# Optimization experiments

Measured on AMD Instinct MI355X. Metric: run time of the kernel, lower is better.

The kernel has to match this reference:

```python
import math
import jax, jax.numpy as jnp
import numpy as np

B, T, D, H, NEXP, TOPK = 2, 1024, 1024, 16, 8, 2
DH = D // H
DFF = 4 * D
NEG = -1e30


def _ln(x, g, b, eps=1e-5):
    m = jnp.mean(x, axis=-1, keepdims=True)
    v = jnp.mean((x - m) ** 2, axis=-1, keepdims=True)
    return (x - m) * jax.lax.rsqrt(v + eps) * g + b


def _build_sin_cos(t, dim, base=10000.0):
    # matches torch build_sin_cos(seq_len, head_dim//2): inv freq over range(0, dim*2, 2)
    pos = jnp.arange(t, dtype=jnp.float32)[:, None]
    inv = jnp.exp(jnp.arange(0, dim * 2, 2, dtype=jnp.float32) * (-math.log(base) / (dim * 2)))
    ang = pos * inv  # (T, dim)
    return jnp.sin(ang), jnp.cos(ang)


def _rope(q, k, sin, cos):
    half = q.shape[-1] // 2
    sin = sin[None, :, None, :]
    cos = cos[None, :, None, :]
    q1, q2 = q[..., :half], q[..., half:]
    k1, k2 = k[..., :half], k[..., half:]
    qr = jnp.concatenate([q1 * cos - q2 * sin, q2 * cos + q1 * sin], axis=-1)
    kr = jnp.concatenate([k1 * cos - k2 * sin, k2 * cos + k1 * sin], axis=-1)
    return qr, kr


def _forward(x, noise, ln1_g, ln1_b, ln2_g, ln2_b, w_qkv, w_proj, w_rl, b_rl, w_rn, b_rn, w1, b1, w2, b2):
    # ---- attention sublayer (LN -> RoPE -> causal attn -> proj, residual) ----
    h = _ln(x, ln1_g, ln1_b)
    qkv = (h @ w_qkv).reshape(B, T, 3, H, DH)
    q, k, v = qkv[:, :, 0], qkv[:, :, 1], qkv[:, :, 2]  # (B,T,H,DH)
    sin, cos = _build_sin_cos(T, DH // 2)
    q, k = _rope(q, k, sin, cos)
    scores = jnp.einsum('bthd,bshd->bhts', q, k) / math.sqrt(DH)
    causal = jnp.tril(jnp.ones((T, T), dtype=bool))
    scores = jnp.where(causal[None, None], scores, NEG)
    attn = jax.nn.softmax(scores, axis=-1)
    ao = jnp.einsum('bhts,bshd->bthd', attn, v).reshape(B, T, D)
    x = x + ao @ w_proj
    # ---- MoE sublayer (noisy top-k router -> capped expert dispatch, residual) ----
    h2 = _ln(x, ln2_g, ln2_b).reshape(B * T, D)
    nz = noise.reshape(B * T, NEXP)
    logits = h2 @ w_rl + b_rl
    noisy = logits + nz * jax.nn.softplus(h2 @ w_rn + b_rn)
    topv, ix = jax.lax.top_k(noisy, TOPK)              # (N,K)
    pk = jax.nn.softmax(topv, axis=-1)                 # softmax over sparse (-inf elsewhere)
    route_p = jnp.sum(pk[..., None] * jax.nn.one_hot(ix, NEXP, dtype=pk.dtype), axis=-2)  # (N,E)
    N = B * T
    cap = int(N * TOPK / NEXP)  # capacity per expert (cap_factor=1.0)
    updates = jnp.zeros((N, D), dtype=x.dtype)
    for i in range(NEXP):
        mask = jnp.any(ix == i, axis=-1)               # (N,) tokens routed to expert i
        sel = jnp.argsort(jnp.logical_not(mask))[:cap]  # first `cap` routed tokens, in order (stable sort)
        valid = mask[sel].astype(x.dtype)              # zero out slots beyond actual routed count
        xe = h2[sel]                                   # (cap, D)
        o = jax.nn.relu(xe @ w1[i] + b1[i]) @ w2[i] + b2[i]
        gate = route_p[sel, i] * valid
        updates = updates.at[sel].add(o * gate[:, None])
    return x + updates.reshape(B, T, D)


def setup_inputs() -> dict:
    key = jax.random.key(0)
    ks = jax.random.split(key, 8)
    s = 0.02
    return {
        'x': jax.random.normal(ks[0], (B, T, D), jnp.float32),
        'noise': jax.random.normal(ks[1], (B, T, NEXP), jnp.float32),
        'ln1_g': jnp.ones((D,), jnp.float32),
        'ln1_b': jnp.zeros((D,), jnp.float32),
        'ln2_g': jnp.ones((D,), jnp.float32),
        'ln2_b': jnp.zeros((D,), jnp.float32),
        'w_qkv': jax.random.normal(ks[2], (D, 3 * D), jnp.float32) * s,
        'w_proj': jax.random.normal(ks[3], (D, D), jnp.float32) * s,
        'w_rl': jax.random.normal(ks[4], (D, NEXP), jnp.float32) * s,
        'b_rl': jnp.zeros((NEXP,), jnp.float32),
        'w_rn': jax.random.normal(ks[5], (D, NEXP), jnp.float32) * s,
        'b_rn': jnp.zeros((NEXP,), jnp.float32),
        'w1': jax.random.normal(ks[6], (NEXP, D, DFF), jnp.float32) * s,
        'b1': jnp.zeros((NEXP, DFF), jnp.float32),
        'w2': jax.random.normal(ks[7], (NEXP, DFF, D), jnp.float32) * s,
        'b2': jnp.zeros((NEXP, D), jnp.float32),
    }


def reference(x, noise, ln1_g, ln1_b, ln2_g, ln2_b, w_qkv, w_proj, w_rl, b_rl, w_rn, b_rn, w1, b1, w2, b2):
    return _forward(x, noise, ln1_g, ln1_b, ln2_g, ln2_b, w_qkv, w_proj, w_rl, b_rl, w_rn, b_rn, w1, b1, w2, b2)
```

## Files before the change

### kernel.cpp

```cpp
#include <hip/hip_runtime.h>


#define TB 1024
#define DD 1024
#define NTOK 2048
#define NEXPERT 8
#define CAPN 512
#define DFF 4096

typedef __attribute__((ext_vector_type(4))) float f32x4;
typedef __attribute__((ext_vector_type(16))) float f32x16;
typedef __attribute__((ext_vector_type(8))) short short8;
typedef __attribute__((ext_vector_type(4))) short short4v;
typedef unsigned short u16;
typedef unsigned int u32;

__device__ __forceinline__ u16 f2bf(float f){
  union { float f; u32 u; } v; v.f = f;
  u32 u = v.u;
  u32 r = (u + 0x7fffu + ((u >> 16) & 1u)) >> 16;
  return (u16)r;
}
__device__ __forceinline__ float bf2f(u16 b){
  union { u32 u; float f; } v; v.u = ((u32)b) << 16;
  return v.f;
}
__device__ __forceinline__ float waveRedSum(float v){
#pragma unroll
  for (int o = 1; o < 64; o <<= 1) v += __shfl_xor(v, o);
  return v;
}

__device__ __forceinline__ void gl16(const u16* g, u16* l){
  __builtin_amdgcn_global_load_lds(
    (const __attribute__((address_space(1))) u32*)g,
    (__attribute__((address_space(3))) u32*)l, 16, 0, 0);
}

__global__ __launch_bounds__(256) void k_prep(
    const float* __restrict__ w_qkv, const float* __restrict__ w_proj,
    const float* __restrict__ w1, const float* __restrict__ w2,
    u16* __restrict__ wqkvT, u16* __restrict__ wprojT,
    u16* __restrict__ w1T, u16* __restrict__ w2T,
    float* __restrict__ st, float* __restrict__ ct,
    const float* __restrict__ x, const float* __restrict__ ln1_g,
    const float* __restrict__ ln1_b, u16* __restrict__ h1)
{
  const int tid = threadIdx.x;
  int bid = blockIdx.x;
  if (bid < 128){
    const int idx = bid * 256 + tid;
    const int t = idx >> 5, i = idx & 31;
    const float inv = expf((float)(2 * i) * (-0.14391157f));
    const float ang = (float)t * inv;
    st[idx] = sinf(ang);
    ct[idx] = cosf(ang);
    return;
  }
  bid -= 128;
  if (bid >= 17408){
    const int row = bid - 17408;
    const int w = tid >> 6, lane = tid & 63;
    const float4 xv = *(const float4*)(x + (long)row*DD + tid*4);
    __shared__ float red[8];
    float s = xv.x + xv.y + xv.z + xv.w;
    s = waveRedSum(s);
    if (lane == 0) red[w] = s;
    __syncthreads();
    const float mean = (red[0]+red[1]+red[2]+red[3]) * (1.f/1024.f);
    const float d0 = xv.x-mean, d1 = xv.y-mean, d2 = xv.z-mean, d3 = xv.w-mean;
    float vs = d0*d0 + d1*d1 + d2*d2 + d3*d3;
    vs = waveRedSum(vs);
    if (lane == 0) red[4+w] = vs;
    __syncthreads();
    const float var = (red[4]+red[5]+red[6]+red[7]) * (1.f/1024.f);
    const float inv = rsqrtf(var + 1e-5f);
    const int c = tid*4;
    short4v p;
    p[0] = (short)f2bf(d0*inv*ln1_g[c+0] + ln1_b[c+0]);
    p[1] = (short)f2bf(d1*inv*ln1_g[c+1] + ln1_b[c+1]);
    p[2] = (short)f2bf(d2*inv*ln1_g[c+2] + ln1_b[c+2]);
    p[3] = (short)f2bf(d3*inv*ln1_g[c+3] + ln1_b[c+3]);
    *(short4v*)(h1 + (long)row*DD + c) = p;
    return;
  }
  const float* src; u16* dst; int K, N, nx, tile;
  long zoff = 0;
  if (bid < 768){
    src = w_qkv; dst = wqkvT; K = DD; N = 3*DD; nx = 48; tile = bid;
  } else if (bid < 768 + 256){
    src = w_proj; dst = wprojT; K = DD; N = DD; nx = 16; tile = bid - 768;
  } else if (bid < 768 + 256 + 8192){
    const int b2 = bid - (768 + 256);
    src = w1; dst = w1T; K = DD; N = DFF; nx = 64; tile = b2 & 1023;
    zoff = (long)(b2 >> 10) * DD * DFF;
  } else {
    const int b2 = bid - (768 + 256 + 8192);
    src = w2; dst = w2T; K = DFF; N = DD; nx = 16; tile = b2 & 1023;
    zoff = (long)(b2 >> 10) * DFF * DD;
  }
  const int n0 = (tile % nx) * 64, k0 = (tile / nx) * 64;
  __shared__ float tb[64][65];
  const int r  = tid >> 2;
  const int c4 = (tid & 3) * 16;
#pragma unroll
  for (int j = 0; j < 4; ++j){
    const float4 v = *(const float4*)(src + zoff + (long)(k0 + r)*N + n0 + c4 + j*4);
    tb[r][c4 + j*4 + 0] = v.x;
    tb[r][c4 + j*4 + 1] = v.y;
    tb[r][c4 + j*4 + 2] = v.z;
    tb[r][c4 + j*4 + 3] = v.w;
  }
  __syncthreads();
  const int n  = tid >> 2;
  const int ks = (tid & 3) * 16;
  short8 o0, o1;
#pragma unroll
  for (int j = 0; j < 8; ++j){
    o0[j] = (short)f2bf(tb[ks + j][n]);
    o1[j] = (short)f2bf(tb[ks + 8 + j][n]);
  }
  u16* dp = dst + zoff + (long)k0*N + (long)(n0 + n)*64 + ks;
  *(short8*)dp = o0;
  *(short8*)(dp + 8) = o1;
}

template<bool GATHER>
__device__ __forceinline__ void gemm_core5(
    const u16* __restrict__ A, int lda, const int* __restrict__ rowlist,
    const u16* __restrict__ Bt, int BN, int K, int kstart, int row0, int col0,
    u16* As0, u16* Bs0, u16* As1, u16* Bs1, f32x16 acc[2][2])
{
  const int tid = threadIdx.x;
  const int lane = tid & 63;
  const int w = tid >> 6;
  const int wr = w >> 1, wc = w & 1;
  const int l31 = lane & 31, l5 = lane >> 5;
  const int rr8 = lane >> 3;
  const int cc8 = ((lane & 7) ^ rr8) * 8;

  const u16* Aq[4];
  const u16* Bq[4];
  int coff[4];
#pragma unroll
  for (int j2 = 0; j2 < 4; ++j2){
    const int j = w + 4*j2;
    long ar;
    if constexpr (GATHER) ar = rowlist[row0 + j*8 + rr8];
    else                  ar = row0 + j*8 + rr8;
    Aq[j2] = A + ar*(long)lda + kstart + cc8;
    Bq[j2] = Bt + (long)kstart*BN + (long)(col0 + j*8 + rr8)*64 + cc8;
    coff[j2] = j*512;
  }

  const int swz = (l31 & 7) * 8;

#define STAGE5(AS, BS, KOFF) \
  _Pragma("unroll") \
  for (int j2 = 0; j2 < 4; ++j2){ \
    gl16(Aq[j2] + (KOFF), (AS) + coff[j2]); \
    gl16(Bq[j2] + (long)(KOFF)*BN, (BS) + coff[j2]); \
  }

#define COMPUTE5(AS, BS) \
  _Pragma("unroll") \
  for (int s = 0; s < 4; ++s){ \
    short8 aF[2], bF[2]; \
    const int cread = ((s*16 + l5*8) ^ swz); \
    _Pragma("unroll") \
    for (int mi = 0; mi < 2; ++mi) \
      aF[mi] = *(const short8*)((AS) + (wr*64 + mi*32 + l31)*64 + cread); \
    _Pragma("unroll") \
    for (int ni = 0; ni < 2; ++ni) \
      bF[ni] = *(const short8*)((BS) + (wc*64 + ni*32 + l31)*64 + cread); \
    _Pragma("unroll") \
    for (int mi = 0; mi < 2; ++mi) \
      _Pragma("unroll") \
      for (int ni = 0; ni < 2; ++ni) \
        acc[mi][ni] = __builtin_amdgcn_mfma_f32_32x32x16_bf16(aF[mi], bF[ni], acc[mi][ni], 0, 0, 0); \
  }

  STAGE5(As0, Bs0, 0)

  for (int k0 = 0; k0 < K; k0 += 128){
    STAGE5(As1, Bs1, k0 + 64)
    asm volatile("s_waitcnt vmcnt(8)" ::: "memory");
    __builtin_amdgcn_s_barrier();
    __builtin_amdgcn_sched_barrier(0);
    COMPUTE5(As0, Bs0)
    __builtin_amdgcn_s_barrier();
    if (k0 + 128 < K){
      STAGE5(As0, Bs0, k0 + 128)
      asm volatile("s_waitcnt vmcnt(8)" ::: "memory");
    } else {
      asm volatile("s_waitcnt vmcnt(0)" ::: "memory");
    }
    __builtin_amdgcn_s_barrier();
    __builtin_amdgcn_sched_barrier(0);
    COMPUTE5(As1, Bs1)
    __builtin_amdgcn_s_barrier();
  }
#undef STAGE5
#undef COMPUTE5
}

#define GEMM_PRE4 \
  __shared__ u16 As0[128*64], Bs0[128*64], As1[128*64], Bs1[128*64]; \
  f32x16 acc[2][2]; \
  _Pragma("unroll") for (int i = 0; i < 2; ++i) \
  _Pragma("unroll") for (int j = 0; j < 2; ++j) \
  _Pragma("unroll") for (int q = 0; q < 16; ++q) acc[i][j][q] = 0.f;

#define GEMM_EPI4_VARS \
  const int lane = threadIdx.x & 63; \
  const int wv = threadIdx.x >> 6;   \
  const int wr = wv >> 1, wc = wv & 1; \
  const int l31 = lane & 31, l5 = lane >> 5;

#define ROW4(mi, r) (row0 + wr*64 + (mi)*32 + ((r)&3) + (((r)>>2)<<3) + l5*4)
#define COL4(ni)    (col0 + wc*64 + (ni)*32 + l31)

__global__ __launch_bounds__(256) void k_gemm_qkv(const u16* __restrict__ h1,
    const u16* __restrict__ wqT, const float* __restrict__ st,
    const float* __restrict__ ct, u16* __restrict__ q_r, u16* __restrict__ k_r,
    u16* __restrict__ v_row)
{
  GEMM_PRE4
  const int id = blockIdx.x;
  const int pcol = id % 24, mt = id / 24;
  const int row0 = mt*128, col0 = pcol*128;
  gemm_core5<false>(h1, DD, nullptr, wqT, 3*DD, DD, 0, row0, col0, As0, Bs0, As1, Bs1, acc);
  GEMM_EPI4_VARS
  if (pcol < 16){
    const int isk = pcol >> 3;
    const int h = (pcol & 7)*2 + wc;
    u16* dstbase = isk ? k_r : q_r;
    const float qs = isk ? 1.f : 0.125f;
#pragma unroll
    for (int mi = 0; mi < 2; ++mi)
#pragma unroll
      for (int r = 0; r < 16; ++r){
        const int rr = ROW4(mi, r);
        const int b = rr >> 10, t = rr & (TB-1);
        const float sv = st[t*32 + l31], cv = ct[t*32 + l31];
        const float a0 = acc[mi][0][r], a1 = acc[mi][1][r];
        const float o1 = (a0*cv - a1*sv) * qs;
        const float o2 = (a1*cv + a0*sv) * qs;
        u16* dst = dstbase + ((long)(b*16 + h)*TB + t)*64 + l31;
        dst[0]  = f2bf(o1);
        dst[32] = f2bf(o2);
      }
  } else {
    const int cb = (pcol - 16)*128 + wc*64;
#pragma unroll
    for (int mi = 0; mi < 2; ++mi)
#pragma unroll
      for (int ni = 0; ni < 2; ++ni)
#pragma unroll
        for (int r = 0; r < 16; ++r){
          const int rr = ROW4(mi, r);
          v_row[(long)rr*DD + cb + ni*32 + l31] = f2bf(acc[mi][ni][r]);
        }
  }
}

__global__ __launch_bounds__(256) void k_vt(const u16* __restrict__ v_row,
    u16* __restrict__ v_t)
{
  __shared__ u16 vt[64*72];
  const int tid = threadIdx.x;
  const int bh = blockIdx.y, b = bh >> 4, h = bh & 15;
  const int t0 = blockIdx.x * 64;
  const int tl = tid >> 2, qq = tid & 3;
  const int t = t0 + tl;
  const long row = (long)(b*TB + t) * DD + h*64;
  const short8 w0 = *(const short8*)(v_row + row + qq*16);
  const short8 w1 = *(const short8*)(v_row + row + qq*16 + 8);
#pragma unroll
  for (int j = 0; j < 8; ++j){
    vt[(qq*16 + j)*72 + tl]     = (u16)w0[j];
    vt[(qq*16 + 8 + j)*72 + tl] = (u16)w1[j];
  }
  __syncthreads();
  const int dh = tid >> 2, seg = tid & 3;
  const short8 r0 = *(const short8*)(vt + dh*72 + seg*16);
  const short8 r1 = *(const short8*)(vt + dh*72 + seg*16 + 8);
  u16* vp = v_t + ((long)bh*64 + dh)*TB + t0 + seg*16;
  *(short8*)vp = r0; *(short8*)(vp + 8) = r1;
}

__global__ __launch_bounds__(512) void k_attn(const u16* __restrict__ q_r,
    const u16* __restrict__ k_r, const u16* __restrict__ v_t,
    u16* __restrict__ aoc, float2* __restrict__ mLc)
{
  const int qt = blockIdx.x, bh = blockIdx.y, ch = blockIdx.z;
  const int kvlen = (qt + 1) * 128;
  const int s_begin = ch * 512;
  if (s_begin >= kvlen) return;
  const int ntile = (min(s_begin + 512, kvlen) - s_begin) >> 6;

  __shared__ u16 K_lds[2][64*64];
  __shared__ u16 V_lds[2][64*64];
  __shared__ u16 P_lds[8][16*80];

  const int tid = threadIdx.x;
  const int w = tid >> 6, lane = tid & 63;
  const int l15 = lane & 15, l4 = lane >> 4;
  const int q0 = qt*128 + w*16;
  u16* P = &P_lds[w][0];

  const int srow = tid >> 3, sslot = tid & 7;
  const u16* kq = k_r + ((long)bh*TB + s_begin + srow)*64 + ((sslot ^ (srow & 7))*8);
  const u16* vq = v_t + ((long)bh*64 + srow)*TB + s_begin + ((sslot ^ (srow & 7))*8);
  u16* kD = &K_lds[0][0] + tid*8;
  u16* vD = &V_lds[0][0] + tid*8;

  const long qoff = ((long)bh*TB + q0 + l15)*64 + l4*8;
  const short8 Qf0 = *(const short8*)(q_r + qoff);
  const short8 Qf1 = *(const short8*)(q_r + qoff + 32);
  const f32x4 fz = {0.f,0.f,0.f,0.f};
  f32x4 O[4];
  float m[4], L[4];
#pragma unroll
  for (int i = 0; i < 4; ++i){ O[i] = fz; m[i] = -1e30f; L[i] = 0.f; }

  gl16(kq, kD);
  gl16(vq, vD);

  for (int t = 0; t < ntile; ++t){
    const int s0 = s_begin + t*64;
    const int cur = t & 1;
    if (t + 1 < ntile){
      gl16(kq + (t+1)*4096, kD + (cur^1)*4096);
      gl16(vq + (t+1)*64,   vD + (cur^1)*4096);
      asm volatile("s_waitcnt vmcnt(2)" ::: "memory");
    } else {
      asm volatile("s_waitcnt vmcnt(0)" ::: "memory");
    }
    __builtin_amdgcn_s_barrier();
    __builtin_amdgcn_sched_barrier(0);
    if (s0 <= q0 + 15){
      const u16* Kb = &K_lds[cur][0];
      const u16* Vb = &V_lds[cur][0];
      f32x4 S[4];
#pragma unroll
      for (int sj = 0; sj < 4; ++sj){
        const int rl = sj*16 + l15;
        const short8 kf0 = *(const short8*)(Kb + rl*64 + ((l4 ^ (rl & 7))*8));
        const short8 kf1 = *(const short8*)(Kb + rl*64 + (((l4 + 4) ^ (rl & 7))*8));
        f32x4 z = fz;
        z = __builtin_amdgcn_mfma_f32_16x16x32_bf16(Qf0, kf0, z, 0, 0, 0);
        z = __builtin_amdgcn_mfma_f32_16x16x32_bf16(Qf1, kf1, z, 0, 0, 0);
        S[sj] = z;
      }
      if (s0 + 63 > q0){
#pragma unroll
        for (int sj = 0; sj < 4; ++sj)
#pragma unroll
          for (int r = 0; r < 4; ++r){
            const int sc = s0 + sj*16 + l15;
            const int qr = q0 + l4*4 + r;
            if (sc > qr) S[sj][r] = -1e30f;
          }
      }
      float vm[4];
#pragma unroll
      for (int r = 0; r < 4; ++r){
        vm[r] = fmaxf(fmaxf(S[0][r], S[1][r]), fmaxf(S[2][r], S[3][r]));
        vm[r] = fmaxf(vm[r], __shfl_xor(vm[r], 1));
        vm[r] = fmaxf(vm[r], __shfl_xor(vm[r], 2));
        vm[r] = fmaxf(vm[r], __shfl_xor(vm[r], 4));
        vm[r] = fmaxf(vm[r], __shfl_xor(vm[r], 8));
      }
      float corr[4], ls[4];
#pragma unroll
      for (int r = 0; r < 4; ++r){
        const float mn = fmaxf(m[r], vm[r]);
        corr[r] = __expf(m[r] - mn);
        m[r] = mn;
        ls[r] = 0.f;
      }
#pragma unroll
      for (int sj = 0; sj < 4; ++sj)
#pragma unroll
        for (int r = 0; r < 4; ++r){
          const float pv = __expf(S[sj][r] - m[r]);
          S[sj][r] = pv;
          ls[r] += pv;
        }
#pragma unroll
      for (int r = 0; r < 4; ++r){
        ls[r] += __shfl_xor(ls[r], 1);
        ls[r] += __shfl_xor(ls[r], 2);
        ls[r] += __shfl_xor(ls[r], 4);
        ls[r] += __shfl_xor(ls[r], 8);
        L[r] = L[r]*corr[r] + ls[r];
      }
#pragma unroll
      for (int nj = 0; nj < 4; ++nj)
#pragma unroll
        for (int r = 0; r < 4; ++r)
          O[nj][r] *= corr[r];
#pragma unroll
      for (int sj = 0; sj < 4; ++sj)
#pragma unroll
        for (int r = 0; r < 4; ++r)
          P[(l4*4 + r)*80 + sj*16 + l15] = f2bf(S[sj][r]);
      asm volatile("s_waitcnt lgkmcnt(0)" ::: "memory");
      __builtin_amdgcn_sched_barrier(0);
      const short8 pf0 = *(const short8*)(P + l15*80 + l4*8);
      const short8 pf1 = *(const short8*)(P + l15*80 + 32 + l4*8);
#pragma unroll
      for (int nj = 0; nj < 4; ++nj){
        const int rl = nj*16 + l15;
        const short8 vf0 = *(const short8*)(Vb + rl*64 + ((l4 ^ (rl & 7))*8));
        const short8 vf1 = *(const short8*)(Vb + rl*64 + (((l4 + 4) ^ (rl & 7))*8));
        O[nj] = __builtin_amdgcn_mfma_f32_16x16x32_bf16(pf0, vf0, O[nj], 0, 0, 0);
        O[nj] = __builtin_amdgcn_mfma_f32_16x16x32_bf16(pf1, vf1, O[nj], 0, 0, 0);
      }
    }
    __builtin_amdgcn_sched_barrier(0);
    __builtin_amdgcn_s_barrier();
  }
  const long obase = ((long)(bh*8 + qt)*2 + ch) * 8192;
#pragma unroll
  for (int nj = 0; nj < 4; ++nj)
#pragma unroll
    for (int r = 0; r < 4; ++r)
      aoc[obase + (long)(w*16 + l4*4 + r)*64 + nj*16 + l15] = f2bf(O[nj][r]);
  if (l15 == 0){
#pragma unroll
    for (int r = 0; r < 4; ++r)
      mLc[((long)(bh*8 + qt)*2 + ch)*128 + w*16 + l4*4 + r] = make_float2(m[r], L[r]);
  }
}

__global__ __launch_bounds__(256) void k_attn_comb(const u16* __restrict__ aoc,
    const float2* __restrict__ mLc, u16* __restrict__ ao)
{
  const int bq = blockIdx.x;
  const int qt = bq & 7, bh = bq >> 3, b = bh >> 4, h = bh & 15;
  const int nc2 = (qt >= 4);
  const int d = threadIdx.x & 63;
  const int r0 = threadIdx.x >> 6;
  const long base = (long)bq * 2 * 8192;
  const long mbase = (long)bq * 2 * 128;
  for (int rp = 0; rp < 32; ++rp){
    const int r = rp*4 + r0;
    const float2 ml0 = mLc[mbase + r];
    float o, Lg;
    if (nc2){
      const float2 ml1 = mLc[mbase + 128 + r];
      const float mg = fmaxf(ml0.x, ml1.x);
      const float w0 = __expf(ml0.x - mg), w1 = __expf(ml1.x - mg);
      o  = w0 * bf2f(aoc[base + (long)r*64 + d]) + w1 * bf2f(aoc[base + 8192 + (long)r*64 + d]);
      Lg = w0 * ml0.y + w1 * ml1.y;
    } else {
      o  = bf2f(aoc[base + (long)r*64 + d]);
      Lg = ml0.y;
    }
    const int t = qt*128 + r;
    ao[((long)b*TB + t)*DD + h*64 + d] = f2bf(o / Lg);
  }
}

__global__ __launch_bounds__(256) void k_gemm_proj(const u16* __restrict__ ao,
    const u16* __restrict__ wpT, const float* __restrict__ x, float* __restrict__ out)
{
  GEMM_PRE4
  const int id = blockIdx.x;
  const int pcol = id % 8, mt = id / 8;
  const int row0 = mt*128, col0 = pcol*128;
  gemm_core5<false>(ao, DD, nullptr, wpT, DD, DD, 0, row0, col0, As0, Bs0, As1, Bs1, acc);
  GEMM_EPI4_VARS
#pragma unroll
  for (int mi = 0; mi < 2; ++mi)
#pragma unroll
    for (int ni = 0; ni < 2; ++ni)
#pragma unroll
      for (int r = 0; r < 16; ++r){
        const int rr = ROW4(mi, r);
        const int cc = COL4(ni);
        out[(long)rr*DD + cc] = x[(long)rr*DD + cc] + acc[mi][ni][r];
      }
}

__global__ __launch_bounds__(256) void k_ln2r(const float* __restrict__ x,
    const float* __restrict__ g, const float* __restrict__ bb,
    const float* __restrict__ w_rl, const float* __restrict__ b_rl,
    const float* __restrict__ w_rn, const float* __restrict__ b_rn,
    const float* __restrict__ noise, u16* __restrict__ h2b,
    int2* __restrict__ tok_e, float2* __restrict__ tok_g, int* __restrict__ slot_of)
{
  const int row = blockIdx.x, tid = threadIdx.x;
  const int w = tid >> 6, lane = tid & 63;
  const float4 xv = *(const float4*)(x + (long)row*DD + tid*4);
  __shared__ float red[8];
  __shared__ float red2[4][16];
  float s = xv.x + xv.y + xv.z + xv.w;
  s = waveRedSum(s);
  if (lane == 0) red[w] = s;
  __syncthreads();
  const float mean = (red[0]+red[1]+red[2]+red[3]) * (1.f/1024.f);
  const float d0 = xv.x-mean, d1 = xv.y-mean, d2 = xv.z-mean, d3 = xv.w-mean;
  float vs = d0*d0 + d1*d1 + d2*d2 + d3*d3;
  vs = waveRedSum(vs);
  if (lane == 0) red[4+w] = vs;
  __syncthreads();
  const float var = (red[4]+red[5]+red[6]+red[7]) * (1.f/1024.f);
  const float inv = rsqrtf(var + 1e-5f);
  const int c = tid*4;
  const float hv[4] = {
    d0*inv*g[c+0] + bb[c+0], d1*inv*g[c+1] + bb[c+1],
    d2*inv*g[c+2] + bb[c+2], d3*inv*g[c+3] + bb[c+3]};
  short4v p;
#pragma unroll
  for (int j = 0; j < 4; ++j) p[j] = (short)f2bf(hv[j]);
  *(short4v*)(h2b + (long)row*DD + c) = p;

  float accl[8] = {0,0,0,0,0,0,0,0};
  float accn[8] = {0,0,0,0,0,0,0,0};
#pragma unroll
  for (int j = 0; j < 4; ++j){
    const int k = c + j;
    const float4 a = *(const float4*)(w_rl + k*8);
    const float4 b = *(const float4*)(w_rl + k*8 + 4);
    accl[0] += hv[j]*a.x; accl[1] += hv[j]*a.y; accl[2] += hv[j]*a.z; accl[3] += hv[j]*a.w;
    accl[4] += hv[j]*b.x; accl[5] += hv[j]*b.y; accl[6] += hv[j]*b.z; accl[7] += hv[j]*b.w;
    const float4 cc = *(const float4*)(w_rn + k*8);
    const float4 d = *(const float4*)(w_rn + k*8 + 4);
    accn[0] += hv[j]*cc.x; accn[1] += hv[j]*cc.y; accn[2] += hv[j]*cc.z; accn[3] += hv[j]*cc.w;
    accn[4] += hv[j]*d.x; accn[5] += hv[j]*d.y; accn[6] += hv[j]*d.z; accn[7] += hv[j]*d.w;
  }
#pragma unroll
  for (int e = 0; e < 8; ++e){ accl[e] = waveRedSum(accl[e]); accn[e] = waveRedSum(accn[e]); }
  if (lane == 0){
#pragma unroll
    for (int e = 0; e < 8; ++e){ red2[w][e] = accl[e]; red2[w][8+e] = accn[e]; }
  }
  __syncthreads();
  if (tid == 0){
    float nv[8];
#pragma unroll
    for (int e = 0; e < 8; ++e){
      const float lr = red2[0][e]+red2[1][e]+red2[2][e]+red2[3][e] + b_rl[e];
      const float lnv = red2[0][8+e]+red2[1][8+e]+red2[2][8+e]+red2[3][8+e] + b_rn[e];
      const float sp = fmaxf(lnv, 0.f) + log1pf(expf(-fabsf(lnv)));
      nv[e] = lr + noise[row*8 + e] * sp;
    }
    int bi = 0; float bvv = nv[0];
#pragma unroll
    for (int e = 1; e < 8; ++e) if (nv[e] > bvv){ bvv = nv[e]; bi = e; }
    int si = (bi == 0) ? 1 : 0;
    float sv = nv[si];
#pragma unroll
    for (int e = 0; e < 8; ++e) if (e != bi && nv[e] > sv){ sv = nv[e]; si = e; }
    const float tt = expf(sv - bvv);
    tok_e[row] = make_int2(bi, si);
    tok_g[row] = make_float2(1.f/(1.f + tt), tt/(1.f + tt));
    slot_of[row*2]     = -1;
    slot_of[row*2 + 1] = -1;
  }
}

__global__ __launch_bounds__(256) void k_assign(const int2* __restrict__ tok_e,
    int* __restrict__ expert_tok, int* __restrict__ slot_of)
{
  const int e = blockIdx.x, tid = threadIdx.x;
  __shared__ int cnt[256];
  expert_tok[e*CAPN + tid] = 0;
  expert_tok[e*CAPN + 256 + tid] = 0;
  int which[8]; int c = 0;
  const int t0 = tid * 8;
#pragma unroll
  for (int j = 0; j < 8; ++j){
    const int2 te = tok_e[t0 + j];
    int wj = -1;
    if (te.x == e) wj = 0; else if (te.y == e) wj = 1;
    which[j] = wj;
    c += (wj >= 0) ? 1 : 0;
  }
  cnt[tid] = c;
  __syncthreads();
  if (tid == 0){
    int run = 0;
    for (int i = 0; i < 256; ++i){ const int v = cnt[i]; cnt[i] = run; run += v; }
  }
  __syncthreads();
  int pos = cnt[tid];
#pragma unroll
  for (int j = 0; j < 8; ++j){
    if (which[j] >= 0){
      if (pos < CAPN){
        expert_tok[e*CAPN + pos] = t0 + j;
        slot_of[(t0 + j)*2 + which[j]] = e*CAPN + pos;
      }
      ++pos;
    }
  }
}

__global__ __launch_bounds__(256) void k_ffn1(const u16* __restrict__ h2b,
    const u16* __restrict__ w1T, const float* __restrict__ b1,
    const int* __restrict__ expert_tok, u16* __restrict__ act)
{
  GEMM_PRE4
  const int id = blockIdx.x;
  const int chunk = (id & 7) * 128 + (id >> 3);
  const int mt = chunk & 3, pcol = (chunk >> 2) & 31, z = chunk >> 7;
  const int row0 = mt*128, col0 = pcol*128;
  gemm_core5<true>(h2b, DD, expert_tok + z*CAPN, w1T + (long)z*DD*DFF, DFF, DD, 0,
                   row0, col0, As0, Bs0, As1, Bs1, acc);
  GEMM_EPI4_VARS
#pragma unroll
  for (int mi = 0; mi < 2; ++mi)
#pragma unroll
    for (int ni = 0; ni < 2; ++ni)
#pragma unroll
      for (int r = 0; r < 16; ++r){
        const int rr = ROW4(mi, r);
        const int cc = COL4(ni);
        const float val = fmaxf(acc[mi][ni][r] + b1[z*DFF + cc], 0.f);
        act[((long)z*CAPN + rr)*DFF + cc] = f2bf(val);
      }
}

__global__ __launch_bounds__(256) void k_ffn2(const u16* __restrict__ act,
    const u16* __restrict__ w2T, u16* __restrict__ partial)
{
  GEMM_PRE4
  const int id = blockIdx.x;
  const int chunk = (id & 7) * 64 + (id >> 3);
  const int ks = chunk & 1, mt = (chunk >> 1) & 3, pcol = (chunk >> 3) & 7, z = chunk >> 6;
  const int row0 = mt*128, col0 = pcol*128;
  gemm_core5<false>(act + (long)z*CAPN*DFF, DFF, nullptr,
                    w2T + (long)z*DFF*DD, DD, 2048, ks*2048,
                    row0, col0, As0, Bs0, As1, Bs1, acc);
  GEMM_EPI4_VARS
  u16* pp = partial + (long)ks*NEXPERT*CAPN*DD;
#pragma unroll
  for (int mi = 0; mi < 2; ++mi)
#pragma unroll
    for (int ni = 0; ni < 2; ++ni)
#pragma unroll
      for (int r = 0; r < 16; ++r){
        const int rr = ROW4(mi, r);
        const int cc = COL4(ni);
        pp[((long)z*CAPN + rr)*DD + cc] = f2bf(acc[mi][ni][r]);
      }
}

__global__ __launch_bounds__(256) void k_combine(float* __restrict__ out,
    const int* __restrict__ slot_of, const float2* __restrict__ tok_g,
    const u16* __restrict__ partial, const float* __restrict__ b2)
{
  const int tok = blockIdx.x, c = threadIdx.x * 4;
  float4 o = *(float4*)(out + (long)tok*DD + c);
  const int2 ss = *(const int2*)(slot_of + tok*2);
  const float2 g = tok_g[tok];
#pragma unroll
  for (int j = 0; j < 2; ++j){
    const int s = j ? ss.y : ss.x;
    const float gw = j ? g.y : g.x;
    if (s >= 0){
      const int e = s >> 9;
      float4 a = *(const float4*)(b2 + e*DD + c);
#pragma unroll
      for (int ks = 0; ks < 2; ++ks){
        const short4v pv = *(const short4v*)(partial + (long)ks*NEXPERT*CAPN*DD + (long)s*DD + c);
        a.x += bf2f((u16)pv[0]); a.y += bf2f((u16)pv[1]);
        a.z += bf2f((u16)pv[2]); a.w += bf2f((u16)pv[3]);
      }
      o.x += gw*a.x; o.y += gw*a.y; o.z += gw*a.z; o.w += gw*a.w;
    }
  }
  *(float4*)(out + (long)tok*DD + c) = o;
}

extern "C" void kernel_launch(void* const* d_in, const int* in_sizes, int n_in,
                              void* d_out, int out_size, void* d_ws, size_t ws_size,
                              hipStream_t stream)
{
  (void)in_sizes; (void)n_in; (void)out_size; (void)ws_size;
  const float* x      = (const float*)d_in[0];
  const float* noise  = (const float*)d_in[1];
  const float* ln1_g  = (const float*)d_in[2];
  const float* ln1_b  = (const float*)d_in[3];
  const float* ln2_g  = (const float*)d_in[4];
  const float* ln2_b  = (const float*)d_in[5];
  const float* w_qkv  = (const float*)d_in[6];
  const float* w_proj = (const float*)d_in[7];
  const float* w_rl   = (const float*)d_in[8];
  const float* b_rl   = (const float*)d_in[9];
  const float* w_rn   = (const float*)d_in[10];
  const float* b_rn   = (const float*)d_in[11];
  const float* w1     = (const float*)d_in[12];
  const float* b1     = (const float*)d_in[13];
  const float* w2     = (const float*)d_in[14];
  const float* b2     = (const float*)d_in[15];
  float* out = (float*)d_out;

  char* p = (char*)d_ws;
  auto carve = [&](size_t bytes) -> void* {
    void* r = (void*)p;
    p += (bytes + 255) & ~(size_t)255;
    return r;
  };
  const size_t SLOT = (size_t)NTOK*DD*2;
  float* sin_t      = (float*)carve((size_t)TB*32*4);
  float* cos_t      = (float*)carve((size_t)TB*32*4);
  char*  region     = (char*)carve(SLOT*8);
  u16*   h1    = (u16*)region;
  u16*   v_row = (u16*)(region + SLOT);
  u16*   q_r   = (u16*)(region + SLOT*4);
  u16*   k_r   = (u16*)(region + SLOT*5);
  u16*   v_t   = (u16*)(region + SLOT*6);
  u16*   ao    = (u16*)(region + SLOT*7);
  u16*   aoc   = (u16*)region;
  float2* mLc  = (float2*)(region + SLOT*2);
  u16*   act   = (u16*)region;
  u16*   h2b        = (u16*)  carve((size_t)NTOK*DD*2);
  int2*  tok_e      = (int2*) carve((size_t)NTOK*8);
  float2* tok_g     = (float2*)carve((size_t)NTOK*8);
  int*   slot_of    = (int*)  carve((size_t)NTOK*2*4);
  int*   expert_tok = (int*)  carve((size_t)NEXPERT*CAPN*4);
  u16*   wqkvT      = (u16*)  carve((size_t)DD*3*DD*2);
  u16*   wprojT     = (u16*)  carve((size_t)DD*DD*2);
  u16*   w1T        = (u16*)  carve((size_t)NEXPERT*DD*DFF*2);
  u16*   w2T        = (u16*)  carve((size_t)NEXPERT*DFF*DD*2);
  u16*   partial    = (u16*)w1T;

  k_prep   <<<19584, 256, 0, stream>>>(w_qkv, w_proj, w1, w2,
                                       wqkvT, wprojT, w1T, w2T, sin_t, cos_t,
                                       x, ln1_g, ln1_b, h1);
  k_gemm_qkv<<<384, 256, 0, stream>>>(h1, wqkvT, sin_t, cos_t, q_r, k_r, v_row);
  k_vt     <<<dim3(16, 32), 256, 0, stream>>>(v_row, v_t);
  k_attn   <<<dim3(8, 32, 2), 512, 0, stream>>>(q_r, k_r, v_t, aoc, mLc);
  k_attn_comb<<<256, 256, 0, stream>>>(aoc, mLc, ao);
  k_gemm_proj<<<128, 256, 0, stream>>>(ao, wprojT, x, out);
  k_ln2r   <<<NTOK, 256, 0, stream>>>(out, ln2_g, ln2_b, w_rl, b_rl, w_rn, b_rn,
                                      noise, h2b, tok_e, tok_g, slot_of);
  k_assign <<<NEXPERT, 256, 0, stream>>>(tok_e, expert_tok, slot_of);
  k_ffn1   <<<1024, 256, 0, stream>>>(h2b, w1T, b1, expert_tok, act);
  k_ffn2   <<<512, 256, 0, stream>>>(act, w2T, partial);
  k_combine<<<NTOK, 256, 0, stream>>>(out, slot_of, tok_g, partial, b2);
}
```

Baseline: 312.3 us.

## Widen weight-transpose tiles and convert to bf16 before staging in LDS

The weight prep kernel now transposes 64x256 tiles per block instead of 64x64, cutting the block count from about 19.6k to 6.5k. Each thread converts fp32 to bf16 while loading, so LDS holds u16 values with a padded stride, which halves shared-memory footprint and traffic. The write-out then gathers 8 k-values per output row into 16-byte stores. This aims to lower launch and scheduling overhead and make the large weight conversion pass more bandwidth-efficient. The risk is LDS bank conflicts on 16-bit strided reads and lower occupancy per block.

Result: no change. 312.7 us (+0.1%).

```diff
diff --git a/kernel.cpp b/kernel.cpp
--- a/kernel.cpp
+++ b/kernel.cpp
@@ -58,8 +58,8 @@
     return;
   }
   bid -= 128;
-  if (bid >= 17408){
-    const int row = bid - 17408;
+  if (bid >= 4352){
+    const int row = bid - 4352;
     const int w = tid >> 6, lane = tid & 63;
     const float4 xv = *(const float4*)(x + (long)row*DD + tid*4);
     __shared__ float red[8];
@@ -84,45 +84,46 @@
     *(short4v*)(h1 + (long)row*DD + c) = p;
     return;
   }
-  const float* src; u16* dst; int K, N, nx, tile;
+  const float* src; u16* dst; int N, nnx, tile;
   long zoff = 0;
-  if (bid < 768){
-    src = w_qkv; dst = wqkvT; K = DD; N = 3*DD; nx = 48; tile = bid;
-  } else if (bid < 768 + 256){
-    src = w_proj; dst = wprojT; K = DD; N = DD; nx = 16; tile = bid - 768;
-  } else if (bid < 768 + 256 + 8192){
-    const int b2 = bid - (768 + 256);
-    src = w1; dst = w1T; K = DD; N = DFF; nx = 64; tile = b2 & 1023;
-    zoff = (long)(b2 >> 10) * DD * DFF;
+  if (bid < 192){
+    src = w_qkv; dst = wqkvT; N = 3*DD; nnx = 12; tile = bid;
+  } else if (bid < 256){
+    src = w_proj; dst = wprojT; N = DD; nnx = 4; tile = bid - 192;
+  } else if (bid < 2304){
+    const int b2 = bid - 256;
+    src = w1; dst = w1T; N = DFF; nnx = 16; tile = b2 & 255;
+    zoff = (long)(b2 >> 8) * DD * DFF;
   } else {
-    const int b2 = bid - (768 + 256 + 8192);
-    src = w2; dst = w2T; K = DFF; N = DD; nx = 16; tile = b2 & 1023;
-    zoff = (long)(b2 >> 10) * DFF * DD;
-  }
-  const int n0 = (tile % nx) * 64, k0 = (tile / nx) * 64;
-  __shared__ float tb[64][65];
-  const int r  = tid >> 2;
-  const int c4 = (tid & 3) * 16;
-#pragma unroll
-  for (int j = 0; j < 4; ++j){
-    const float4 v = *(const float4*)(src + zoff + (long)(k0 + r)*N + n0 + c4 + j*4);
-    tb[r][c4 + j*4 + 0] = v.x;
-    tb[r][c4 + j*4 + 1] = v.y;
-    tb[r][c4 + j*4 + 2] = v.z;
-    tb[r][c4 + j*4 + 3] = v.w;
+    const int b2 = bid - 2304;
+    src = w2; dst = w2T; N = DD; nnx = 4; tile = b2 & 255;
+    zoff = (long)(b2 >> 8) * DFF * DD;
+  }
+  const int n0 = (tile % nnx) * 256, k0 = (tile / nnx) * 64;
+
+  __shared__ u16 tb[64*258];
+#pragma unroll
+  for (int i = 0; i < 16; ++i){
+    const int r = i*4 + (tid >> 6);
+    const int c = (tid & 63) * 4;
+    const float4 v = *(const float4*)(src + zoff + (long)(k0 + r)*N + n0 + c);
+    const u32 lo = (u32)f2bf(v.x) | ((u32)f2bf(v.y) << 16);
+    const u32 hi = (u32)f2bf(v.z) | ((u32)f2bf(v.w) << 16);
+    *(u32*)(tb + r*258 + c)     = lo;
+    *(u32*)(tb + r*258 + c + 2) = hi;
   }
   __syncthreads();
-  const int n  = tid >> 2;
-  const int ks = (tid & 3) * 16;
-  short8 o0, o1;
-#pragma unroll
-  for (int j = 0; j < 8; ++j){
-    o0[j] = (short)f2bf(tb[ks + j][n]);
-    o1[j] = (short)f2bf(tb[ks + 8 + j][n]);
-  }
-  u16* dp = dst + zoff + (long)k0*N + (long)(n0 + n)*64 + ks;
-  *(short8*)dp = o0;
-  *(short8*)(dp + 8) = o1;
+  const int koct = tid & 7;
+  u16* dpb = dst + zoff + (long)k0*N + (long)n0*64 + koct*8;
+#pragma unroll
+  for (int q = 0; q < 8; ++q){
+    const int n = q*32 + (tid >> 3);
+    short8 o;
+#pragma unroll
+    for (int j = 0; j < 8; ++j)
+      o[j] = (short)tb[(koct*8 + j)*258 + n];
+    *(short8*)(dpb + (long)n*64) = o;
+  }
 }
 
 template<bool GATHER>
@@ -730,9 +731,9 @@
   u16*   w2T        = (u16*)  carve((size_t)NEXPERT*DFF*DD*2);
   u16*   partial    = (u16*)w1T;
 
-  k_prep   <<<19584, 256, 0, stream>>>(w_qkv, w_proj, w1, w2,
-                                       wqkvT, wprojT, w1T, w2T, sin_t, cos_t,
-                                       x, ln1_g, ln1_b, h1);
+  k_prep   <<<6528, 256, 0, stream>>>(w_qkv, w_proj, w1, w2,
+                                      wqkvT, wprojT, w1T, w2T, sin_t, cos_t,
+                                      x, ln1_g, ln1_b, h1);
   k_gemm_qkv<<<384, 256, 0, stream>>>(h1, wqkvT, sin_t, cos_t, q_r, k_r, v_row);
   k_vt     <<<dim3(16, 32), 256, 0, stream>>>(v_row, v_t);
   k_attn   <<<dim3(8, 32, 2), 512, 0, stream>>>(q_r, k_r, v_t, aoc, mLc);
```
